# Performance work log

Measured on AMD Instinct MI355X. Metric: run time of the kernel, lower is better.

The kernel has to match this reference:

```python
import jax, jax.numpy as jnp
import numpy as np

N_SIGMA = 3
FG_W = 1.0
W_INST, W_VAR, W_SEED = 1.0, 10.0, 1.0
N_IDS = 16  # instance ids 1..16; id 0 = background
B, C, D, H, W = 4, 7, 32, 192, 192


def setup_inputs() -> dict:
    key = jax.random.key(0)
    k1, k2, k3, k4 = jax.random.split(key, 4)
    prediction = jax.random.normal(k1, (B, C, D, H, W), dtype=jnp.float32)
    instances = jax.random.randint(k2, (B, D, H, W), 0, N_IDS + 1, dtype=jnp.int32)
    labels = jax.random.randint(k3, (B, D, H, W), 0, 2, dtype=jnp.int32)
    center_images = jax.random.randint(k4, (B, D, H, W), 0, 2) > 0
    # coordinate buffer, pixel_{x,y,z}=1, grid dims == volume dims
    xm = jnp.broadcast_to(jnp.linspace(0.0, 1.0, W).reshape(1, 1, W), (D, H, W))
    ym = jnp.broadcast_to(jnp.linspace(0.0, 1.0, H).reshape(1, H, 1), (D, H, W))
    zm = jnp.broadcast_to(jnp.linspace(0.0, 1.0, D).reshape(D, 1, 1), (D, H, W))
    xyzm = jnp.stack([xm, ym, zm], 0).astype(jnp.float32)  # [3,D,H,W]
    return {"prediction": prediction, "instances": instances, "labels": labels,
            "center_images": center_images, "xyzm": xyzm}


def _lovasz_hinge(logits, gt):
    # logits, gt: flat [N]; gt in {0,1} float. Lovasz grad is detached (Variable(grad) in torch impl).
    signs = 2.0 * gt - 1.0
    errors = 1.0 - logits * signs
    order = jnp.argsort(-errors)  # descending
    errors_sorted = errors[order]
    gt_sorted = gt[order]
    gts = gt_sorted.sum()
    intersection = gts - jnp.cumsum(gt_sorted)
    union = gts + jnp.cumsum(1.0 - gt_sorted)
    jaccard = 1.0 - intersection / union
    grad = jnp.concatenate([jaccard[:1], jaccard[1:] - jaccard[:-1]])
    return jnp.dot(jax.nn.relu(errors_sorted), jax.lax.stop_gradient(grad))


def reference(prediction, instances, labels, center_images, xyzm):
    bsz = prediction.shape[0]
    dhw = prediction.shape[2] * prediction.shape[3] * prediction.shape[4]
    spatial_emb = jnp.tanh(prediction[:, :3]) + xyzm[None]             # [B,3,D,H,W]
    sigma = prediction[:, 3:3 + N_SIGMA]                               # [B,3,D,H,W]
    seed_map = jax.nn.sigmoid(prediction[:, 3 + N_SIGMA])              # [B,D,H,W]

    bg_seed = jnp.sum(jnp.where(labels == 0, seed_map ** 2, 0.0), axis=(1, 2, 3))  # [B]

    ids = jnp.arange(1, N_IDS + 1)

    def per_instance(se_b, sigma_b, seed_b, inst_b, iid):
        m = (inst_b == iid).astype(jnp.float32)                         # [D,H,W]
        cnt = m.sum()
        exists = cnt > 0
        safe = jnp.maximum(cnt, 1.0)
        center = jnp.sum(xyzm * m[None], axis=(1, 2, 3)) / safe         # [3]
        s_mean = jnp.sum(sigma_b * m[None], axis=(1, 2, 3)) / safe      # [n_sigma]
        var = jnp.sum(((sigma_b - jax.lax.stop_gradient(s_mean)[:, None, None, None]) ** 2) * m[None]) / (N_SIGMA * safe)
        s_exp = jnp.exp(s_mean * 10.0)[:, None, None, None]
        dist = jnp.exp(-jnp.sum(((se_b - center[:, None, None, None]) ** 2) * s_exp, axis=0))  # [D,H,W]
        inst_l = _lovasz_hinge((dist * 2.0 - 1.0).reshape(-1), m.reshape(-1))
        seed_l = FG_W * jnp.sum(((seed_b - jax.lax.stop_gradient(dist)) ** 2) * m)
        z = jnp.float32(0.0)
        return (jnp.where(exists, var, z), jnp.where(exists, inst_l, z),
                jnp.where(exists, seed_l, z), exists.astype(jnp.float32))

    def per_batch(se_b, sigma_b, seed_b, inst_b):
        v, il, sl, ex = jax.vmap(per_instance, in_axes=(None, None, None, None, 0))(
            se_b, sigma_b, seed_b, inst_b, ids)
        obj = ex.sum()
        denom = jnp.maximum(obj, 1.0)
        return v.sum() / denom, il.sum() / denom, sl.sum()

    var_b, inst_lb, seed_lb = jax.vmap(per_batch)(spatial_emb, sigma, seed_map, instances)
    seed_total = (seed_lb + bg_seed) / dhw
    loss_inst = inst_lb.sum() * W_INST / bsz
    loss_var = var_b.sum() * W_VAR / bsz
    loss_seed = seed_total.sum() * W_SEED / bsz
    loss_sum = loss_inst + loss_var + loss_seed + prediction.sum() * 0.0
    return jnp.stack([loss_inst, loss_var, loss_seed, loss_sum])
```

## Files before the change

kernel.cpp:

```cpp
#include <hip/hip_runtime.h>

#define NID  16
#define BB   4
#define HH   192
#define WW   192
#define DHW  1179648
#define KB   256

#define P1_ROWS   24
#define P1_ITERS  72

#define P3_CHUNKS 192
#define P3_CHUNK  6144
#define SUBT      6
#define SUBN      1024
#define SUBIT     4

#define WS_STATS 0
#define WS_BG8   512
#define WS_SEED8 544
#define WS_INSTL 576
#define WS_HIST  640
#define WS_TOTAL (640 + 64*2*KB)

__device__ __forceinline__ float ftanh(float x) {
    float t = __expf(2.f * x);
    return 1.f - 2.f / (t + 1.f);
}
__device__ __forceinline__ float fsigmoid(float x) {
    return 1.f / (1.f + __expf(-x));
}
__device__ __forceinline__ float wred(float v) {
    for (int off = 32; off > 0; off >>= 1) v += __shfl_down(v, off, 64);
    return v;
}
__device__ __forceinline__ void xyz_of(int v, float& x, float& y, float& z) {
    int w = v % WW;
    int t = v / WW;
    int h = t % HH;
    int d = t / HH;
    x = (float)w * (1.f / 191.f);
    y = (float)h * (1.f / 191.f);
    z = (float)d * (1.f / 31.f);
}

#define REP8(M) M(0) M(1) M(2) M(3) M(4) M(5) M(6) M(7)

__global__ __launch_bounds__(256) void pass1_stats(
    const float* __restrict__ pred, const int* __restrict__ inst,
    const int* __restrict__ labels, float* __restrict__ ws)
{
    __shared__ float part[128];
    const int b    = blockIdx.y;
    const int tid  = threadIdx.x;
    const int wv   = tid >> 6;
    const int lane = tid & 63;
    const int idb0 = (wv & 1) * 8;

    const float* p3 = pred + (size_t)(b * 7 + 3) * DHW;
    const int*   ib = inst   + (size_t)b * DHW;
    const int*   lb = labels + (size_t)b * DHW;
    const int row0 = blockIdx.x * P1_ROWS;

    if (wv < 2) {
        unsigned G00=0u,G01=0u,G02=0u,G03=0u,G04=0u,G05=0u,G06=0u,G07=0u;
        unsigned G10=0u,G11=0u,G12=0u,G13=0u,G14=0u,G15=0u,G16=0u,G17=0u;
        float bgacc = 0.f;
        for (int it = 0; it < P1_ITERS; ++it) {
            const int seg = it % 3, r = it / 3;
            const int row = row0 + r;
            const int w   = seg * 64 + lane;
            const int v   = row * WW + w;
            const int id  = ib[v];
            if (wv == 0) {
                const float seed = fsigmoid(p3[3 * DHW + v]);
                if (lb[v] == 0) bgacc += seed * seed;
            }
            const unsigned p0 = (unsigned)w | (1u << 17);
            const unsigned p1 = (unsigned)(row % HH) | ((unsigned)(row / HH) << 17);
            const int idx = id - 1 - idb0;
            #define GEO(Q) { const bool e = (idx == Q); \
                             G0##Q += e ? p0 : 0u; G1##Q += e ? p1 : 0u; }
            REP8(GEO)
            #undef GEO
        }
        #define GRED(Q) { \
            float c  = wred((float)(G0##Q >> 17)); \
            float sx = wred((float)(G0##Q & 0x1FFFFu) * (1.f / 191.f)); \
            float sy = wred((float)(G1##Q & 0x1FFFFu) * (1.f / 191.f)); \
            float sz = wred((float)(G1##Q >> 17)      * (1.f / 31.f)); \
            if (lane == 0) { float* pp = &part[(idb0 + Q) * 8]; \
                             pp[0] = c; pp[1] = sx; pp[2] = sy; pp[3] = sz; } }
        REP8(GRED)
        #undef GRED
        if (wv == 0) {
            const float r = wred(bgacc);
            if (lane == 0) atomicAdd(&ws[WS_BG8 + b * 8 + (blockIdx.x & 7)], r);
        }
    } else {
        float SA0=0.f,SA1=0.f,SA2=0.f,SA3=0.f,SA4=0.f,SA5=0.f,SA6=0.f,SA7=0.f;
        float SB0=0.f,SB1=0.f,SB2=0.f,SB3=0.f,SB4=0.f,SB5=0.f,SB6=0.f,SB7=0.f;
        float SC0=0.f,SC1=0.f,SC2=0.f,SC3=0.f,SC4=0.f,SC5=0.f,SC6=0.f,SC7=0.f;
        float SD0=0.f,SD1=0.f,SD2=0.f,SD3=0.f,SD4=0.f,SD5=0.f,SD6=0.f,SD7=0.f;
        for (int it = 0; it < P1_ITERS; ++it) {
            const int seg = it % 3, r = it / 3;
            const int v   = (row0 + r) * WW + seg * 64 + lane;
            const int id  = ib[v];
            const float s0 = p3[v], s1 = p3[DHW + v], s2 = p3[2 * DHW + v];
            const float sq = s0 * s0 + s1 * s1 + s2 * s2;
            const int idx = id - 1 - idb0;
            #define SIG(Q) { const float m = (idx == Q) ? 1.f : 0.f; \
                SA##Q = fmaf(m, s0, SA##Q); SB##Q = fmaf(m, s1, SB##Q); \
                SC##Q = fmaf(m, s2, SC##Q); SD##Q = fmaf(m, sq, SD##Q); }
            REP8(SIG)
            #undef SIG
        }
        #define SRED(Q) { \
            float r0 = wred(SA##Q), r1 = wred(SB##Q); \
            float r2 = wred(SC##Q), r3 = wred(SD##Q); \
            if (lane == 0) { float* pp = &part[(idb0 + Q) * 8 + 4]; \
                             pp[0] = r0; pp[1] = r1; pp[2] = r2; pp[3] = r3; } }
        REP8(SRED)
        #undef SRED
    }
    __syncthreads();
    if (tid < 128) {
        const float pv = part[tid];
        if (pv != 0.f) atomicAdd(&ws[WS_STATS + b * 128 + tid], pv);
    }
}

__global__ __launch_bounds__(256) void pass3_hist(
    const float* __restrict__ pred, const int* __restrict__ inst,
    float* __restrict__ ws)
{
    __shared__ float4 sev[SUBN];
    __shared__ unsigned cntFB[2][NID][KB + 1];
    __shared__ float ctrs[NID][8];
    __shared__ float sred[4];

    const int b   = blockIdx.y;
    const int tid = threadIdx.x;
    const int rep = (tid >> 5) & 1;
    const int rot = tid & 15;

    for (int i = tid; i < 2 * NID * (KB + 1); i += 256) ((unsigned*)cntFB)[i] = 0u;
    if (tid < NID) {
        const float* s = ws + WS_STATS + (size_t)(b * NID + tid) * 8;
        const float cnt = s[0];
        const float safe = fmaxf(cnt, 1.f);
        const float m0 = s[4] / safe, m1 = s[5] / safe, m2 = s[6] / safe;
        ctrs[tid][0] = s[1] / safe;
        ctrs[tid][1] = s[2] / safe;
        ctrs[tid][2] = s[3] / safe;
        ctrs[tid][3] = __expf(10.f * m0);
        ctrs[tid][4] = __expf(10.f * m1);
        ctrs[tid][5] = __expf(10.f * m2);
        ctrs[tid][6] = 0.f;
        ctrs[tid][7] = (cnt > 0.f) ? 1.f : 0.f;
    }
    __syncthreads();

    const float* pb = pred + (size_t)b * 7 * DHW;
    const int*   ib = inst + (size_t)b * DHW;

    float sacc = 0.f;
    const int base0 = blockIdx.x * P3_CHUNK;

    for (int sub = 0; sub < SUBT; ++sub) {
        const int vb = base0 + sub * SUBN;
        for (int it = 0; it < SUBIT; ++it) {
            const int i = it * 256 + tid;
            const int v = vb + i;
            float x, y, z; xyz_of(v, x, y, z);
            const float se0 = ftanh(pb[v])           + x;
            const float se1 = ftanh(pb[DHW + v])     + y;
            const float se2 = ftanh(pb[2 * DHW + v]) + z;
            const float seed = fsigmoid(pb[6 * DHW + v]);
            const unsigned id = (unsigned)ib[v];
            const unsigned sw = (__float_as_uint(seed) & ~0xFFu) | id;
            sev[i] = make_float4(se0, se1, se2, __uint_as_float(sw));
        }
        __syncthreads();
        for (int p = 0; p < 4; ++p) {
            float cx[4], cy[4], cz[4], e0[4], e1[4], e2[4];
            int iidq[4];
            #pragma unroll
            for (int j = 0; j < 4; ++j) {
                const int iid = (p * 4 + j + rot) & 15;
                iidq[j] = iid;
                cx[j] = ctrs[iid][0]; cy[j] = ctrs[iid][1]; cz[j] = ctrs[iid][2];
                e0[j] = ctrs[iid][3]; e1[j] = ctrs[iid][4]; e2[j] = ctrs[iid][5];
            }
            for (int it = 0; it < SUBIT; ++it) {
                const int i = it * 256 + tid;
                const float4 sv = sev[i];
                const unsigned sw = __float_as_uint(sv.w);
                const int id = (int)(sw & 0xFFu);
                const float seed = sv.w;
                #pragma unroll
                for (int j = 0; j < 4; ++j) {
                    const float d0 = sv.x - cx[j];
                    const float d1 = sv.y - cy[j];
                    const float d2 = sv.z - cz[j];
                    const float q2 = d0 * d0 * e0[j] + d1 * d1 * e1[j] + d2 * d2 * e2[j];
                    const float dist = __expf(-q2);
                    const bool m = (id == iidq[j] + 1);
                    const float e = m ? (2.f - 2.f * dist) : (2.f * dist);
                    int k = (int)(e * 128.f);
                    k = min(max(k, 0), KB - 1);
                    const unsigned val = m ? 1u : (k ? 0x10000u : 0u);
                    if (m) { const float ds = seed - dist; sacc += ds * ds; }
                    if (val) atomicAdd(&cntFB[rep][iidq[j]][k], val);
                }
            }
        }
        __syncthreads();
    }

    float* gh = ws + WS_HIST;
    for (int i = tid; i < NID * KB; i += 256) {
        const int iid = i >> 8, k = i & (KB - 1);
        const unsigned c = cntFB[0][iid][k] + cntFB[1][iid][k];
        float* basep = gh + (size_t)(b * NID + iid) * 2 * KB;
        const float cf = (float)(c & 0xFFFFu);
        const float cb = (float)(c >> 16);
        if (cf != 0.f) atomicAdd(&basep[k], cf);
        if (cb != 0.f) atomicAdd(&basep[KB + k], cb);
    }
    float v = sacc;
    for (int off = 32; off > 0; off >>= 1) v += __shfl_down(v, off, 64);
    if ((tid & 63) == 0) sred[tid >> 6] = v;
    __syncthreads();
    if (tid == 0)
        atomicAdd(&ws[WS_SEED8 + b * 8 + (blockIdx.x & 7)],
                  sred[0] + sred[1] + sred[2] + sred[3]);
}

__global__ __launch_bounds__(256) void pass4_lovasz(float* __restrict__ ws)
{
    const int t = blockIdx.x;
    const int j = threadIdx.x;
    __shared__ float sF[KB], sB[KB];
    __shared__ double red[KB];

    const float P = ws[WS_STATS + t * 8];
    const float* gh = ws + WS_HIST + (size_t)t * 2 * KB;

    const int k = KB - 1 - j;
    const float nF = gh[k], nB = gh[KB + k];
    const float mid = ((float)k + 0.5f) * (1.f / 128.f);
    const float rF = nF * mid, rB = nB * mid;

    sF[j] = nF; sB[j] = nB;
    __syncthreads();
    for (int off = 1; off < KB; off <<= 1) {
        float a = 0.f, c = 0.f;
        if (j >= off) { a = sF[j - off]; c = sB[j - off]; }
        __syncthreads();
        sF[j] += a; sB[j] += c;
        __syncthreads();
    }
    double contrib = 0.0;
    if (P > 0.f) {
        const double Bb = (double)sB[j] - (double)nB;
        const double U0 = (double)P + Bb;
        const double Fafter = (double)sF[j];
        contrib = (double)rF / U0
                + (double)rB * ((double)P - Fafter) / (U0 * (U0 + (double)nB));
    }
    red[j] = contrib;
    __syncthreads();
    for (int off = KB / 2; off > 0; off >>= 1) {
        if (j < off) red[j] += red[j + off];
        __syncthreads();
    }
    if (j == 0) ws[WS_INSTL + t] = (float)red[0];
}

__global__ void pass5_final(const float* __restrict__ ws, float* __restrict__ out)
{
    const int t = threadIdx.x;
    __shared__ float pl[3][4];
    if (t < 4) {
        float obj = 0.f, v = 0.f, i2 = 0.f;
        for (int i = 0; i < NID; ++i) {
            const int u = t * NID + i;
            const float* s = ws + WS_STATS + (size_t)u * 8;
            const float cnt = s[0];
            i2 += ws[WS_INSTL + u];
            if (cnt > 0.f) {
                obj += 1.f;
                const float m0 = s[4] / cnt, m1 = s[5] / cnt, m2 = s[6] / cnt;
                v += (s[7] - cnt * (m0 * m0 + m1 * m1 + m2 * m2)) / (3.f * cnt);
            }
        }
        float sb = 0.f, bg = 0.f;
        for (int j = 0; j < 8; ++j) {
            sb += ws[WS_SEED8 + t * 8 + j];
            bg += ws[WS_BG8   + t * 8 + j];
        }
        const float denom = fmaxf(obj, 1.f);
        pl[0][t] = i2 / denom;
        pl[1][t] = v / denom;
        pl[2][t] = (sb + bg) / (float)DHW;
    }
    __syncthreads();
    if (t == 0) {
        const float linst = (pl[0][0] + pl[0][1] + pl[0][2] + pl[0][3]) * (1.0f / BB);
        const float lvar  = (pl[1][0] + pl[1][1] + pl[1][2] + pl[1][3]) * (10.0f / BB);
        const float lseed = (pl[2][0] + pl[2][1] + pl[2][2] + pl[2][3]) * (1.0f / BB);
        out[0] = linst;
        out[1] = lvar;
        out[2] = lseed;
        out[3] = linst + lvar + lseed;
    }
}

extern "C" void kernel_launch(void* const* d_in, const int* in_sizes, int n_in,
                              void* d_out, int out_size, void* d_ws, size_t ws_size,
                              hipStream_t stream)
{
    const float* pred   = (const float*)d_in[0];
    const int*   inst   = (const int*)  d_in[1];
    const int*   labels = (const int*)  d_in[2];
    float* ws  = (float*)d_ws;
    float* out = (float*)d_out;

    hipMemsetAsync(d_ws, 0, (size_t)WS_TOTAL * sizeof(float), stream);

    dim3 grid1(256, BB);
    dim3 grid3(P3_CHUNKS, BB);
    pass1_stats<<<grid1, 256, 0, stream>>>(pred, inst, labels, ws);
    pass3_hist <<<grid3, 256, 0, stream>>>(pred, inst, ws);
    pass4_lovasz<<<64, KB, 0, stream>>>(ws);
    pass5_final<<<1, 64, 0, stream>>>(ws, out);
}
```

Baseline: 337.4 us.

## Expand Gaussian distance into FMA polynomial with exp2 and fuse final reduction kernel

The per-instance squared distance is expanded into a quadratic in the voxel embedding, with coefficients precomputed per instance and pre-scaled by log2(e) and a +8 offset. The inner loop then needs only FMAs plus one exp2 that directly yields the histogram bin times 256. Separately, the final loss kernel is folded into the Lovasz kernel using a last-block atomic counter, which removes one kernel launch. The expanded quadratic form can lose precision through cancellation when embeddings are far from centers.

```diff
diff --git a/kernel.cpp b/kernel.cpp
--- a/kernel.cpp
+++ b/kernel.cpp
@@ -20,8 +20,11 @@
 #define WS_BG8   512
 #define WS_SEED8 544
 #define WS_INSTL 576
-#define WS_HIST  640
-#define WS_TOTAL (640 + 64*2*KB)
+#define WS_CTR   640
+#define WS_HIST  648
+#define WS_TOTAL (648 + 64*2*KB)
+
+#define LOG2E 1.44269504088896f
 
 __device__ __forceinline__ float ftanh(float x) {
     float t = __expf(2.f * x);
@@ -150,13 +153,17 @@
         const float cnt = s[0];
         const float safe = fmaxf(cnt, 1.f);
         const float m0 = s[4] / safe, m1 = s[5] / safe, m2 = s[6] / safe;
-        ctrs[tid][0] = s[1] / safe;
-        ctrs[tid][1] = s[2] / safe;
-        ctrs[tid][2] = s[3] / safe;
-        ctrs[tid][3] = __expf(10.f * m0);
-        ctrs[tid][4] = __expf(10.f * m1);
-        ctrs[tid][5] = __expf(10.f * m2);
-        ctrs[tid][6] = 0.f;
+        const float cx = s[1] / safe, cy = s[2] / safe, cz = s[3] / safe;
+        const float e0 = __expf(10.f * m0);
+        const float e1 = __expf(10.f * m1);
+        const float e2 = __expf(10.f * m2);
+        ctrs[tid][0] = 2.f * LOG2E * e0 * cx;
+        ctrs[tid][1] = 2.f * LOG2E * e1 * cy;
+        ctrs[tid][2] = 2.f * LOG2E * e2 * cz;
+        ctrs[tid][3] = -LOG2E * e0;
+        ctrs[tid][4] = -LOG2E * e1;
+        ctrs[tid][5] = -LOG2E * e2;
+        ctrs[tid][6] = 8.f - LOG2E * (e0 * cx * cx + e1 * cy * cy + e2 * cz * cz);
         ctrs[tid][7] = (cnt > 0.f) ? 1.f : 0.f;
     }
     __syncthreads();
@@ -183,14 +190,15 @@
         }
         __syncthreads();
         for (int p = 0; p < 4; ++p) {
-            float cx[4], cy[4], cz[4], e0[4], e1[4], e2[4];
-            int iidq[4];
+            float b0[4], b1[4], b2[4], a0[4], a1[4], a2[4], cc[4];
+            int ip1[4], iidq[4];
             #pragma unroll
             for (int j = 0; j < 4; ++j) {
                 const int iid = (p * 4 + j + rot) & 15;
-                iidq[j] = iid;
-                cx[j] = ctrs[iid][0]; cy[j] = ctrs[iid][1]; cz[j] = ctrs[iid][2];
-                e0[j] = ctrs[iid][3]; e1[j] = ctrs[iid][4]; e2[j] = ctrs[iid][5];
+                iidq[j] = iid; ip1[j] = iid + 1;
+                b0[j] = ctrs[iid][0]; b1[j] = ctrs[iid][1]; b2[j] = ctrs[iid][2];
+                a0[j] = ctrs[iid][3]; a1[j] = ctrs[iid][4]; a2[j] = ctrs[iid][5];
+                cc[j] = ctrs[iid][6];
             }
             for (int it = 0; it < SUBIT; ++it) {
                 const int i = it * 256 + tid;
@@ -198,19 +206,20 @@
                 const unsigned sw = __float_as_uint(sv.w);
                 const int id = (int)(sw & 0xFFu);
                 const float seed = sv.w;
+                const float vx = sv.x, vy = sv.y, vz = sv.z;
+                const float vx2 = vx * vx, vy2 = vy * vy, vz2 = vz * vz;
                 #pragma unroll
                 for (int j = 0; j < 4; ++j) {
-                    const float d0 = sv.x - cx[j];
-                    const float d1 = sv.y - cy[j];
-                    const float d2 = sv.z - cz[j];
-                    const float q2 = d0 * d0 * e0[j] + d1 * d1 * e1[j] + d2 * d2 * e2[j];
-                    const float dist = __expf(-q2);
-                    const bool m = (id == iidq[j] + 1);
-                    const float e = m ? (2.f - 2.f * dist) : (2.f * dist);
-                    int k = (int)(e * 128.f);
+                    float t = fmaf(a0[j], vx2, fmaf(b0[j], vx, cc[j]));
+                    t = fmaf(a1[j], vy2, fmaf(b1[j], vy, t));
+                    t = fmaf(a2[j], vz2, fmaf(b2[j], vz, t));
+                    const float t256 = exp2f(t);
+                    const bool m = (id == ip1[j]);
+                    const float kf = m ? (256.f - t256) : t256;
+                    int k = (int)kf;
                     k = min(max(k, 0), KB - 1);
                     const unsigned val = m ? 1u : (k ? 0x10000u : 0u);
-                    if (m) { const float ds = seed - dist; sacc += ds * ds; }
+                    if (m) { const float ds = seed - t256 * (1.f / 256.f); sacc += ds * ds; }
                     if (val) atomicAdd(&cntFB[rep][iidq[j]][k], val);
                 }
             }
@@ -237,12 +246,15 @@
                   sred[0] + sred[1] + sred[2] + sred[3]);
 }
 
-__global__ __launch_bounds__(256) void pass4_lovasz(float* __restrict__ ws)
+__global__ __launch_bounds__(256) void pass4_lovasz(float* __restrict__ ws,
+                                                    float* __restrict__ out)
 {
     const int t = blockIdx.x;
     const int j = threadIdx.x;
     __shared__ float sF[KB], sB[KB];
     __shared__ double red[KB];
+    __shared__ int lastBlk;
+    __shared__ float pl[3][4];
 
     const float P = ws[WS_STATS + t * 8];
     const float* gh = ws + WS_HIST + (size_t)t * 2 * KB;
@@ -275,17 +287,20 @@
         if (j < off) red[j] += red[j + off];
         __syncthreads();
     }
-    if (j == 0) ws[WS_INSTL + t] = (float)red[0];
-}
-
-__global__ void pass5_final(const float* __restrict__ ws, float* __restrict__ out)
-{
-    const int t = threadIdx.x;
-    __shared__ float pl[3][4];
-    if (t < 4) {
+    if (j == 0) {
+        ws[WS_INSTL + t] = (float)red[0];
+        __threadfence();
+        const unsigned old = atomicAdd((unsigned*)&ws[WS_CTR], 1u);
+        lastBlk = (old == 63u) ? 1 : 0;
+    }
+    __syncthreads();
+    if (!lastBlk) return;
+    __threadfence();
+
+    if (j < 4) {
         float obj = 0.f, v = 0.f, i2 = 0.f;
         for (int i = 0; i < NID; ++i) {
-            const int u = t * NID + i;
+            const int u = j * NID + i;
             const float* s = ws + WS_STATS + (size_t)u * 8;
             const float cnt = s[0];
             i2 += ws[WS_INSTL + u];
@@ -296,17 +311,17 @@
             }
         }
         float sb = 0.f, bg = 0.f;
-        for (int j = 0; j < 8; ++j) {
-            sb += ws[WS_SEED8 + t * 8 + j];
-            bg += ws[WS_BG8   + t * 8 + j];
+        for (int q = 0; q < 8; ++q) {
+            sb += ws[WS_SEED8 + j * 8 + q];
+            bg += ws[WS_BG8   + j * 8 + q];
         }
         const float denom = fmaxf(obj, 1.f);
-        pl[0][t] = i2 / denom;
-        pl[1][t] = v / denom;
-        pl[2][t] = (sb + bg) / (float)DHW;
-    }
-    __syncthreads();
-    if (t == 0) {
+        pl[0][j] = i2 / denom;
+        pl[1][j] = v / denom;
+        pl[2][j] = (sb + bg) / (float)DHW;
+    }
+    __syncthreads();
+    if (j == 0) {
         const float linst = (pl[0][0] + pl[0][1] + pl[0][2] + pl[0][3]) * (1.0f / BB);
         const float lvar  = (pl[1][0] + pl[1][1] + pl[1][2] + pl[1][3]) * (10.0f / BB);
         const float lseed = (pl[2][0] + pl[2][1] + pl[2][2] + pl[2][3]) * (1.0f / BB);
@@ -333,6 +348,5 @@
     dim3 grid3(P3_CHUNKS, BB);
     pass1_stats<<<grid1, 256, 0, stream>>>(pred, inst, labels, ws);
     pass3_hist <<<grid3, 256, 0, stream>>>(pred, inst, ws);
-    pass4_lovasz<<<64, KB, 0, stream>>>(ws);
-    pass5_final<<<1, 64, 0, stream>>>(ws, out);
-}
+    pass4_lovasz<<<64, KB, 0, stream>>>(ws, out);
+}
```

Measured after the change: 366.0 us. 1.08x slower.
